# Performance work log

Hardware: AMD Instinct MI355X
Metric: run time of the kernel (lower is better)

## Reference

```python
import jax, jax.numpy as jnp
import numpy as np

N_NODES = 100000
N_EDGES = 6400000
D_FEAT = 128
HIDDEN = 16


def _gcn_conv(x, row, col, W, b, n):
    # PyG GCNConv: add self-loops, symmetric norm, message from row -> aggregated at col
    h = x @ W  # [N, out]
    loop = jnp.arange(n, dtype=row.dtype)
    r = jnp.concatenate([row, loop])
    c = jnp.concatenate([col, loop])
    ones = jnp.ones(r.shape[0], dtype=x.dtype)
    deg = jax.ops.segment_sum(ones, c, num_segments=n)  # in-degree incl. self-loop
    dinv = jnp.where(deg > 0, jax.lax.rsqrt(deg), 0.0)
    norm = dinv[r] * dinv[c]  # [E+N]
    msg = h[r] * norm[:, None]  # [E+N, out]
    out = jax.ops.segment_sum(msg, c, num_segments=n)
    return out + b


def setup_inputs() -> dict:
    key = jax.random.key(0)
    ks = jax.random.split(key, 8)
    x = jax.random.normal(ks[0], (N_NODES, D_FEAT), dtype=jnp.float32)
    edge_attr = jax.random.normal(ks[1], (N_EDGES, 1), dtype=jnp.float32)
    edge_row = jnp.sort(jax.random.randint(ks[2], (N_EDGES,), 0, N_NODES, dtype=jnp.int32)).astype(jnp.int64)
    edge_col = jax.random.randint(ks[3], (N_EDGES,), 0, N_NODES, dtype=jnp.int32).astype(jnp.int64)
    W1 = jax.random.normal(ks[4], (D_FEAT + 1, HIDDEN), dtype=jnp.float32) * (1.0 / np.sqrt(D_FEAT + 1))
    b1 = jnp.zeros((HIDDEN,), dtype=jnp.float32)
    W2 = jax.random.normal(ks[5], (HIDDEN, 1), dtype=jnp.float32) * (1.0 / np.sqrt(HIDDEN))
    b2 = jnp.zeros((1,), dtype=jnp.float32)
    return {"x": x, "edge_attr": edge_attr, "edge_row": edge_row, "edge_col": edge_col,
            "W1": W1, "b1": b1, "W2": W2, "b2": b2}


def reference(x, edge_attr, edge_row, edge_col, W1, b1, W2, b2):
    n = x.shape[0]
    # the original Python loop == segment-sum of edge_attr by source node (rows are sorted)
    x_edge = jax.ops.segment_sum(edge_attr, edge_row, num_segments=n)  # [N, 1]
    h = jnp.concatenate([x, x_edge], axis=1)  # [N, D+1]
    h = _gcn_conv(h, edge_row, edge_col, W1, b1, n)
    h = jax.nn.relu(h)
    # dropout is identity in eval mode
    out = _gcn_conv(h, edge_row, edge_col, W2, b2, n)  # [N, 1]
    return out
```

## Files before the change

kernel.cpp:

```cpp
#include <hip/hip_runtime.h>


#define D_FEAT 128
#define HIDDEN 16
#define TILE 8192
#define CAP 17408u
#define FXS 262144.0f
#define FXSI 3.814697265625e-06f

__device__ inline float bf2f(unsigned short u) {
    union { unsigned x; float f; } t; t.x = ((unsigned)u) << 16; return t.f;
}

__global__ __launch_bounds__(256) void k_init(float* xe, unsigned* gcur, int n, int nb) {
    int t = blockIdx.x * 256 + threadIdx.x;
    if (t < n) xe[t] = 0.f;
    if (t < nb) gcur[t * 16] = (unsigned)t * CAP;
}

__global__ __launch_bounds__(1024) void k_sortplace(const int* __restrict__ row,
                                                    const int* __restrict__ col,
                                                    const float* __restrict__ ea,
                                                    float* __restrict__ xe,
                                                    unsigned* __restrict__ gcur,
                                                    unsigned* __restrict__ ebufP,
                                                    int ne, int nb) {
    __shared__ unsigned stage[TILE];
    __shared__ unsigned short sbuck[TILE];
    __shared__ unsigned h[512], base_[512], cursor[512], gb_[512];
    __shared__ unsigned wsum[8];
    int tid = threadIdx.x;
    int lane = tid & 63;
    int w = tid >> 6;
    int tile0 = blockIdx.x * TILE;
    int cnt_t = min(TILE, ne - tile0);
    if (tid < 512) h[tid] = 0u;
    __syncthreads();
    int e0 = tile0 + tid * 8;
    int rr[8], cc[8];
    float aa[8];
    if (e0 + 7 < ne) {
        int4 r0 = *(const int4*)&row[e0];
        int4 r1 = *(const int4*)&row[e0 + 4];
        int4 c0 = *(const int4*)&col[e0];
        int4 c1 = *(const int4*)&col[e0 + 4];
        float4 a0 = *(const float4*)&ea[e0];
        float4 a1 = *(const float4*)&ea[e0 + 4];
        rr[0] = r0.x; rr[1] = r0.y; rr[2] = r0.z; rr[3] = r0.w;
        rr[4] = r1.x; rr[5] = r1.y; rr[6] = r1.z; rr[7] = r1.w;
        cc[0] = c0.x; cc[1] = c0.y; cc[2] = c0.z; cc[3] = c0.w;
        cc[4] = c1.x; cc[5] = c1.y; cc[6] = c1.z; cc[7] = c1.w;
        aa[0] = a0.x; aa[1] = a0.y; aa[2] = a0.z; aa[3] = a0.w;
        aa[4] = a1.x; aa[5] = a1.y; aa[6] = a1.z; aa[7] = a1.w;
    } else {
        #pragma unroll
        for (int k = 0; k < 8; ++k) {
            int e = e0 + k;
            if (e < ne) { rr[k] = row[e]; cc[k] = col[e]; aa[k] = ea[e]; }
            else        { rr[k] = -1; cc[k] = 0; aa[k] = 0.f; }
        }
    }
    #pragma unroll
    for (int k = 0; k < 8; ++k)
        if (rr[k] >= 0) atomicAdd(&h[cc[k] >> 8], 1u);
    int r_first = rr[0];
    float run = aa[0], lead = 0.f;
    #pragma unroll
    for (int k = 1; k < 8; ++k) {
        if (rr[k] == rr[k - 1]) run += aa[k];
        else {
            if (rr[k - 1] == r_first) lead = run;
            else if (rr[k - 1] >= 0) unsafeAtomicAdd(&xe[rr[k - 1]], run);
            run = aa[k];
        }
    }
    int r_last = rr[7];
    float trail = run;
    bool puref = (r_first == r_last);
    int rl_prev = __shfl_up(r_last, 1);
    bool m = (lane > 0) && (r_first == rl_prev);
    float s = trail;
    int f = (puref && m) ? 0 : 1;
    #pragma unroll
    for (int d = 1; d < 64; d <<= 1) {
        float su = __shfl_up(s, d);
        int fu = __shfl_up(f, d);
        if (lane >= d) {
            if (!f) s += su;
            f = f | fu;
        }
    }
    float o_prev = __shfl_up(s, 1);
    float inflow = m ? o_prev : 0.f;
    int rf_next = __shfl_down(r_first, 1);
    bool chain_end = (lane == 63) || (rf_next != r_last);
    if (!puref && r_first >= 0) unsafeAtomicAdd(&xe[r_first], lead + inflow);
    if (chain_end && r_last >= 0)
        unsafeAtomicAdd(&xe[r_last], trail + (puref ? inflow : 0.f));
    __syncthreads();
    unsigned hv = 0, sh = 0;
    if (tid < 512) {
        hv = h[tid];
        sh = hv;
        #pragma unroll
        for (int d = 1; d < 64; d <<= 1) {
            unsigned u = __shfl_up(sh, d);
            if (lane >= d) sh += u;
        }
        if (lane == 63) wsum[w] = sh;
    }
    __syncthreads();
    if (tid < 512) {
        unsigned woff = 0;
        #pragma unroll
        for (int i = 0; i < 8; ++i) woff += (i < w) ? wsum[i] : 0u;
        unsigned ex = sh + woff - hv;
        base_[tid] = ex;
        cursor[tid] = ex;
        if (tid < nb && hv) gb_[tid] = atomicAdd(&gcur[tid * 16], hv);
    }
    __syncthreads();
    #pragma unroll
    for (int k = 0; k < 8; ++k) {
        if (rr[k] >= 0) {
            int b = cc[k] >> 8;
            unsigned p = atomicAdd(&cursor[b], 1u);
            stage[p] = (((unsigned)(cc[k] & 255)) << 24) | (unsigned)rr[k];
            sbuck[p] = (unsigned short)b;
        }
    }
    __syncthreads();
    for (int t = tid; t < cnt_t; t += 1024) {
        unsigned b = sbuck[t];
        unsigned pos = gb_[b] + ((unsigned)t - base_[b]);
        if (pos < (b + 1u) * CAP) ebufP[pos] = stage[t];
    }
}

__global__ __launch_bounds__(512) void k_deghist(const unsigned* __restrict__ gcur,
                                                 const unsigned* __restrict__ ebufP,
                                                 unsigned* __restrict__ deg,
                                                 unsigned* __restrict__ stG, int n) {
    __shared__ unsigned dg[256];
    __shared__ unsigned wsum[4];
    int tid = threadIdx.x, b = blockIdx.x, lane = tid & 63;
    if (tid < 256) dg[tid] = 0u;
    __syncthreads();
    unsigned base = (unsigned)b * CAP;
    unsigned m = min(gcur[b * 16] - base, CAP);
    unsigned i = tid;
    for (; i + 1536 < m; i += 2048) {
        unsigned pk0 = ebufP[base + i];
        unsigned pk1 = ebufP[base + i + 512];
        unsigned pk2 = ebufP[base + i + 1024];
        unsigned pk3 = ebufP[base + i + 1536];
        atomicAdd(&dg[pk0 >> 24], 1u);
        atomicAdd(&dg[pk1 >> 24], 1u);
        atomicAdd(&dg[pk2 >> 24], 1u);
        atomicAdd(&dg[pk3 >> 24], 1u);
    }
    for (; i < m; i += 512) atomicAdd(&dg[ebufP[base + i] >> 24], 1u);
    __syncthreads();
    unsigned dval = 0, s = 0;
    if (tid < 256) {
        dval = dg[tid];
        s = dval;
        #pragma unroll
        for (int d = 1; d < 64; d <<= 1) {
            unsigned uu = __shfl_up(s, d);
            if (lane >= d) s += uu;
        }
        if (lane == 63) wsum[tid >> 6] = s;
    }
    __syncthreads();
    if (tid < 256) {
        int w = tid >> 6;
        unsigned woff = 0;
        #pragma unroll
        for (int i2 = 0; i2 < 4; ++i2) woff += (i2 < w) ? wsum[i2] : 0u;
        unsigned ex = s + woff - dval;
        int v = b * 256 + tid;
        if (v < n) { deg[v] = dval; stG[v] = base + ex; }
    }
}

__global__ __launch_bounds__(256) void k_gemm1(const float* __restrict__ x,
                                               const float* __restrict__ xe,
                                               const unsigned* __restrict__ deg,
                                               const float* __restrict__ W1,
                                               float* __restrict__ g,
                                               unsigned short* __restrict__ gb, int n) {
    __shared__ float WsT[16 * 132];
    __shared__ float xs[64 * 132];
    int tid = threadIdx.x;
    for (int idx = tid; idx < 129 * 16; idx += 256) {
        int k = idx >> 4, j = idx & 15;
        WsT[j * 132 + k] = W1[idx];
    }
    int n0 = blockIdx.x * 64;
    const float4* x4 = (const float4*)x;
    for (int idx = tid; idx < 64 * 32; idx += 256) {
        int r = idx >> 5, c = idx & 31;
        float4 v = (n0 + r < n) ? x4[(size_t)(n0 + r) * 32 + c]
                                : make_float4(0.f, 0.f, 0.f, 0.f);
        *(float4*)&xs[r * 132 + c * 4] = v;
    }
    if (tid < 64) {
        int r = tid;
        xs[r * 132 + 128] = (n0 + r < n) ? xe[n0 + r] : 0.f;
    }
    __syncthreads();
    int j  = tid & 15;
    int nb = tid >> 4;
    const float* wrow = &WsT[j * 132];
    for (int rep = 0; rep < 4; ++rep) {
        int nl = nb + (rep << 4);
        int node = n0 + nl;
        const float* xrow = &xs[nl * 132];
        float acc = 0.f;
        #pragma unroll
        for (int k = 0; k < 128; k += 4) {
            float4 xv = *(const float4*)&xrow[k];
            float4 wv = *(const float4*)&wrow[k];
            acc += xv.x * wv.x;
            acc += xv.y * wv.y;
            acc += xv.z * wv.z;
            acc += xv.w * wv.w;
        }
        acc += xrow[128] * wrow[128];
        if (node < n) {
            float v = acc * rsqrtf((float)deg[node] + 1.0f);
            g[(size_t)node * 16 + j] = v;
            union { float f; unsigned u; } cv; cv.f = v;
            unsigned r16 = (cv.u + 0x7FFFu + ((cv.u >> 16) & 1u)) >> 16;
            gb[(size_t)node * 16 + j] = (unsigned short)r16;
        }
    }
}

__global__ __launch_bounds__(512) void k_agg1s(const unsigned* __restrict__ gcur,
                                               const unsigned* __restrict__ ebufP,
                                               const unsigned* __restrict__ deg,
                                               const unsigned* __restrict__ stG,
                                               const unsigned* __restrict__ gu,
                                               const float* __restrict__ g,
                                               const float* __restrict__ b1,
                                               const float* __restrict__ W2,
                                               float* __restrict__ g2, int n) {
    __shared__ unsigned sorted[CAP];
    __shared__ unsigned dg[256], st[256], cur[256];
    int tid = threadIdx.x, b = blockIdx.x;
    unsigned base = (unsigned)b * CAP;
    unsigned m = min(gcur[b * 16] - base, CAP);
    if (tid < 256) {
        int v = b * 256 + tid;
        unsigned dval = (v < n) ? deg[v] : 0u;
        unsigned sv   = (v < n) ? stG[v] - base : 0u;
        dg[tid] = dval;
        st[tid] = sv;
        cur[tid] = sv;
    }
    __syncthreads();
    unsigned i = tid;
    for (; i + 1536 < m; i += 2048) {
        unsigned pk0 = ebufP[base + i];
        unsigned pk1 = ebufP[base + i + 512];
        unsigned pk2 = ebufP[base + i + 1024];
        unsigned pk3 = ebufP[base + i + 1536];
        unsigned p0 = atomicAdd(&cur[pk0 >> 24], 1u);
        unsigned p1 = atomicAdd(&cur[pk1 >> 24], 1u);
        unsigned p2 = atomicAdd(&cur[pk2 >> 24], 1u);
        unsigned p3 = atomicAdd(&cur[pk3 >> 24], 1u);
        if (p0 < CAP) sorted[p0] = pk0 & 0xFFFFFFu;
        if (p1 < CAP) sorted[p1] = pk1 & 0xFFFFFFu;
        if (p2 < CAP) sorted[p2] = pk2 & 0xFFFFFFu;
        if (p3 < CAP) sorted[p3] = pk3 & 0xFFFFFFu;
    }
    for (; i < m; i += 512) {
        unsigned pk = ebufP[base + i];
        unsigned p = atomicAdd(&cur[pk >> 24], 1u);
        if (p < CAP) sorted[p] = pk & 0xFFFFFFu;
    }
    __syncthreads();
    const uint4* gu4 = (const uint4*)gu;
    int grp = tid >> 4;
    int u = tid & 1;
    int oct = (tid >> 1) & 7;
    float4 bbA = ((const float4*)b1)[2 * u];
    float4 bbB = ((const float4*)b1)[2 * u + 1];
    float4 wwA = ((const float4*)W2)[2 * u];
    float4 wwB = ((const float4*)W2)[2 * u + 1];
    for (int it = 0; it < 8; ++it) {
        int c = it * 32 + grp;
        int v = b * 256 + c;
        if (v >= n) break;
        unsigned s0 = st[c], e0 = s0 + dg[c];
        float a0 = 0.f, a1 = 0.f, a2 = 0.f, a3 = 0.f;
        float a4 = 0.f, a5 = 0.f, a6 = 0.f, a7 = 0.f;
        float c0 = 0.f, c1 = 0.f, c2 = 0.f, c3 = 0.f;
        float c4 = 0.f, c5 = 0.f, c6 = 0.f, c7 = 0.f;
        unsigned q = s0 + oct;
        for (; q + 8 < e0; q += 16) {
            uint4 w0 = gu4[(size_t)sorted[q] * 2 + u];
            uint4 w1 = gu4[(size_t)sorted[q + 8] * 2 + u];
            a0 += bf2f((unsigned short)w0.x); a1 += bf2f((unsigned short)(w0.x >> 16));
            a2 += bf2f((unsigned short)w0.y); a3 += bf2f((unsigned short)(w0.y >> 16));
            a4 += bf2f((unsigned short)w0.z); a5 += bf2f((unsigned short)(w0.z >> 16));
            a6 += bf2f((unsigned short)w0.w); a7 += bf2f((unsigned short)(w0.w >> 16));
            c0 += bf2f((unsigned short)w1.x); c1 += bf2f((unsigned short)(w1.x >> 16));
            c2 += bf2f((unsigned short)w1.y); c3 += bf2f((unsigned short)(w1.y >> 16));
            c4 += bf2f((unsigned short)w1.z); c5 += bf2f((unsigned short)(w1.z >> 16));
            c6 += bf2f((unsigned short)w1.w); c7 += bf2f((unsigned short)(w1.w >> 16));
        }
        for (; q < e0; q += 8) {
            uint4 w0 = gu4[(size_t)sorted[q] * 2 + u];
            a0 += bf2f((unsigned short)w0.x); a1 += bf2f((unsigned short)(w0.x >> 16));
            a2 += bf2f((unsigned short)w0.y); a3 += bf2f((unsigned short)(w0.y >> 16));
            a4 += bf2f((unsigned short)w0.z); a5 += bf2f((unsigned short)(w0.z >> 16));
            a6 += bf2f((unsigned short)w0.w); a7 += bf2f((unsigned short)(w0.w >> 16));
        }
        a0 += c0; a1 += c1; a2 += c2; a3 += c3;
        a4 += c4; a5 += c5; a6 += c6; a7 += c7;
        #pragma unroll
        for (int d = 2; d <= 8; d <<= 1) {
            a0 += __shfl_xor(a0, d, 16);
            a1 += __shfl_xor(a1, d, 16);
            a2 += __shfl_xor(a2, d, 16);
            a3 += __shfl_xor(a3, d, 16);
            a4 += __shfl_xor(a4, d, 16);
            a5 += __shfl_xor(a5, d, 16);
            a6 += __shfl_xor(a6, d, 16);
            a7 += __shfl_xor(a7, d, 16);
        }
        float di = rsqrtf((float)dg[c] + 1.0f);
        float4 gA = ((const float4*)g)[(size_t)v * 4 + 2 * u];
        float4 gB = ((const float4*)g)[(size_t)v * 4 + 2 * u + 1];
        float v0 = fmaxf(di * (gA.x + a0) + bbA.x, 0.f);
        float v1 = fmaxf(di * (gA.y + a1) + bbA.y, 0.f);
        float v2 = fmaxf(di * (gA.z + a2) + bbA.z, 0.f);
        float v3 = fmaxf(di * (gA.w + a3) + bbA.w, 0.f);
        float v4 = fmaxf(di * (gB.x + a4) + bbB.x, 0.f);
        float v5 = fmaxf(di * (gB.y + a5) + bbB.y, 0.f);
        float v6 = fmaxf(di * (gB.z + a6) + bbB.z, 0.f);
        float v7 = fmaxf(di * (gB.w + a7) + bbB.w, 0.f);
        float prd = v0 * wwA.x + v1 * wwA.y + v2 * wwA.z + v3 * wwA.w
                  + v4 * wwB.x + v5 * wwB.y + v6 * wwB.z + v7 * wwB.w;
        prd += __shfl_xor(prd, 1, 16);
        if ((tid & 15) == 0) g2[v] = prd * di;
    }
}

__global__ __launch_bounds__(512) void k_agg2i(const unsigned* __restrict__ gcur,
                                               const unsigned* __restrict__ ebufP,
                                               const unsigned* __restrict__ deg,
                                               const float* __restrict__ g2,
                                               const float* __restrict__ b2,
                                               float* __restrict__ out, int n) {
    __shared__ int acc2[256];
    int tid = threadIdx.x, b = blockIdx.x;
    if (tid < 256) acc2[tid] = 0;
    __syncthreads();
    unsigned base = (unsigned)b * CAP;
    unsigned m = min(gcur[b * 16] - base, CAP);
    unsigned mt = m & ~3u;
    const uint4* eb4 = (const uint4*)(ebufP + base);
    for (unsigned t = tid; t * 4 + 3 < m; t += 512) {
        uint4 pk = eb4[t];
        float v0 = g2[pk.x & 0xFFFFFFu];
        float v1 = g2[pk.y & 0xFFFFFFu];
        float v2 = g2[pk.z & 0xFFFFFFu];
        float v3 = g2[pk.w & 0xFFFFFFu];
        atomicAdd(&acc2[pk.x >> 24], __float2int_rn(v0 * FXS));
        atomicAdd(&acc2[pk.y >> 24], __float2int_rn(v1 * FXS));
        atomicAdd(&acc2[pk.z >> 24], __float2int_rn(v2 * FXS));
        atomicAdd(&acc2[pk.w >> 24], __float2int_rn(v3 * FXS));
    }
    for (unsigned t = mt + tid; t < m; t += 512) {
        unsigned pk = ebufP[base + t];
        atomicAdd(&acc2[pk >> 24], __float2int_rn(g2[pk & 0xFFFFFFu] * FXS));
    }
    __syncthreads();
    if (tid < 256) {
        int v = b * 256 + tid;
        if (v < n) {
            float a = (float)acc2[tid] * FXSI;
            float di = rsqrtf((float)deg[v] + 1.0f);
            out[v] = di * (g2[v] + a) + b2[0];
        }
    }
}

extern "C" void kernel_launch(void* const* d_in, const int* in_sizes, int n_in,
                              void* d_out, int out_size, void* d_ws, size_t ws_size,
                              hipStream_t stream) {
    const float* x   = (const float*)d_in[0];
    const float* ea  = (const float*)d_in[1];
    const int*   row = (const int*)d_in[2];
    const int*   col = (const int*)d_in[3];
    const float* W1  = (const float*)d_in[4];
    const float* b1  = (const float*)d_in[5];
    const float* W2  = (const float*)d_in[6];
    const float* b2  = (const float*)d_in[7];
    float* out = (float*)d_out;

    int n  = in_sizes[0] / D_FEAT;
    int ne = in_sizes[2];
    int nb = (n + 255) >> 8;

    float* ws   = (float*)d_ws;
    float* xe   = ws;
    float* g    = ws + (size_t)n;
    float* g2   = ws + (size_t)17 * n;
    unsigned short* gbuf = (unsigned short*)(ws + (size_t)18 * n);
    unsigned* deg  = (unsigned*)(ws + (size_t)26 * n);
    unsigned* stG  = deg + (size_t)n;
    unsigned* gcur = stG + (size_t)n;
    unsigned* ebufP = gcur + (size_t)nb * 16;

    dim3 blk(256);
    int g_node = (n + 255) / 256;
    int g_tile = (ne + TILE - 1) / TILE;
    int g_gemm = (n + 63) / 64;

    k_init<<<g_node, blk, 0, stream>>>(xe, gcur, n, nb);
    k_sortplace<<<g_tile, 1024, 0, stream>>>(row, col, ea, xe, gcur, ebufP, ne, nb);
    k_deghist<<<nb, 512, 0, stream>>>(gcur, ebufP, deg, stG, n);
    k_gemm1<<<g_gemm, blk, 0, stream>>>(x, xe, deg, W1, g, gbuf, n);
    k_agg1s<<<nb, 512, 0, stream>>>(gcur, ebufP, deg, stG, (const unsigned*)gbuf, g, b1, W2, g2, n);
    k_agg2i<<<nb, 512, 0, stream>>>(gcur, ebufP, deg, g2, b2, out, n);
}
```

Baseline: 257.0 us.

## Run the x@W1 GEMM concurrently with edge bucketing in one fused kernel

The edge sort/place kernel and the 128-wide part of the first GEMM now share one launch, with blocks assigned by bid%3 to either sorting or a 64-node GEMM tile. The GEMM result no longer depends on the degree, so the x_edge column, the degree normalisation and the bf16 packing move into the degree-histogram kernel as a per-node epilogue. This drops one launch and lets the memory-bound GEMM overlap the atomic-heavy sort. The cost is a union shared-memory footprint sized for the larger role, an extra read-modify-write pass over g, and role imbalance if the two grid counts differ.

```diff
diff --git a/kernel.cpp b/kernel.cpp
--- a/kernel.cpp
+++ b/kernel.cpp
@@ -18,133 +18,200 @@
     if (t < nb) gcur[t * 16] = (unsigned)t * CAP;
 }
 
-__global__ __launch_bounds__(1024) void k_sortplace(const int* __restrict__ row,
-                                                    const int* __restrict__ col,
-                                                    const float* __restrict__ ea,
-                                                    float* __restrict__ xe,
-                                                    unsigned* __restrict__ gcur,
-                                                    unsigned* __restrict__ ebufP,
-                                                    int ne, int nb) {
-    __shared__ unsigned stage[TILE];
-    __shared__ unsigned short sbuck[TILE];
-    __shared__ unsigned h[512], base_[512], cursor[512], gb_[512];
-    __shared__ unsigned wsum[8];
+__global__ __launch_bounds__(1024) void k_sortgemm(const int* __restrict__ row,
+                                                   const int* __restrict__ col,
+                                                   const float* __restrict__ ea,
+                                                   float* __restrict__ xe,
+                                                   unsigned* __restrict__ gcur,
+                                                   unsigned* __restrict__ ebufP,
+                                                   int ne, int nb,
+                                                   const float* __restrict__ x,
+                                                   const float* __restrict__ W1,
+                                                   float* __restrict__ g, int n) {
+    __shared__ union {
+        struct {
+            unsigned stage[TILE];
+            unsigned short sbuck[TILE];
+            unsigned h[512], base_[512], cursor[512], gb_[512];
+            unsigned wsum[8];
+        } sp;
+        struct {
+            float WsT[16 * 132];
+            float xs[64 * 132];
+        } gm;
+    } u;
+    int bid = blockIdx.x;
     int tid = threadIdx.x;
-    int lane = tid & 63;
-    int w = tid >> 6;
-    int tile0 = blockIdx.x * TILE;
-    int cnt_t = min(TILE, ne - tile0);
-    if (tid < 512) h[tid] = 0u;
-    __syncthreads();
-    int e0 = tile0 + tid * 8;
-    int rr[8], cc[8];
-    float aa[8];
-    if (e0 + 7 < ne) {
-        int4 r0 = *(const int4*)&row[e0];
-        int4 r1 = *(const int4*)&row[e0 + 4];
-        int4 c0 = *(const int4*)&col[e0];
-        int4 c1 = *(const int4*)&col[e0 + 4];
-        float4 a0 = *(const float4*)&ea[e0];
-        float4 a1 = *(const float4*)&ea[e0 + 4];
-        rr[0] = r0.x; rr[1] = r0.y; rr[2] = r0.z; rr[3] = r0.w;
-        rr[4] = r1.x; rr[5] = r1.y; rr[6] = r1.z; rr[7] = r1.w;
-        cc[0] = c0.x; cc[1] = c0.y; cc[2] = c0.z; cc[3] = c0.w;
-        cc[4] = c1.x; cc[5] = c1.y; cc[6] = c1.z; cc[7] = c1.w;
-        aa[0] = a0.x; aa[1] = a0.y; aa[2] = a0.z; aa[3] = a0.w;
-        aa[4] = a1.x; aa[5] = a1.y; aa[6] = a1.z; aa[7] = a1.w;
+    int role = bid % 3;
+    if (role == 0) {
+        int sb = bid / 3;
+        int ntile = (ne + TILE - 1) / TILE;
+        if (sb >= ntile) return;
+        unsigned* stage = u.sp.stage;
+        unsigned short* sbuck = u.sp.sbuck;
+        unsigned* h = u.sp.h;
+        unsigned* base_ = u.sp.base_;
+        unsigned* cursor = u.sp.cursor;
+        unsigned* gb_ = u.sp.gb_;
+        unsigned* wsum = u.sp.wsum;
+        int lane = tid & 63;
+        int w = tid >> 6;
+        int tile0 = sb * TILE;
+        int cnt_t = min(TILE, ne - tile0);
+        if (tid < 512) h[tid] = 0u;
+        __syncthreads();
+        int e0 = tile0 + tid * 8;
+        int rr[8], cc[8];
+        float aa[8];
+        if (e0 + 7 < ne) {
+            int4 r0 = *(const int4*)&row[e0];
+            int4 r1 = *(const int4*)&row[e0 + 4];
+            int4 c0 = *(const int4*)&col[e0];
+            int4 c1 = *(const int4*)&col[e0 + 4];
+            float4 a0 = *(const float4*)&ea[e0];
+            float4 a1 = *(const float4*)&ea[e0 + 4];
+            rr[0] = r0.x; rr[1] = r0.y; rr[2] = r0.z; rr[3] = r0.w;
+            rr[4] = r1.x; rr[5] = r1.y; rr[6] = r1.z; rr[7] = r1.w;
+            cc[0] = c0.x; cc[1] = c0.y; cc[2] = c0.z; cc[3] = c0.w;
+            cc[4] = c1.x; cc[5] = c1.y; cc[6] = c1.z; cc[7] = c1.w;
+            aa[0] = a0.x; aa[1] = a0.y; aa[2] = a0.z; aa[3] = a0.w;
+            aa[4] = a1.x; aa[5] = a1.y; aa[6] = a1.z; aa[7] = a1.w;
+        } else {
+            #pragma unroll
+            for (int k = 0; k < 8; ++k) {
+                int e = e0 + k;
+                if (e < ne) { rr[k] = row[e]; cc[k] = col[e]; aa[k] = ea[e]; }
+                else        { rr[k] = -1; cc[k] = 0; aa[k] = 0.f; }
+            }
+        }
+        #pragma unroll
+        for (int k = 0; k < 8; ++k)
+            if (rr[k] >= 0) atomicAdd(&h[cc[k] >> 8], 1u);
+        int r_first = rr[0];
+        float run = aa[0], lead = 0.f;
+        #pragma unroll
+        for (int k = 1; k < 8; ++k) {
+            if (rr[k] == rr[k - 1]) run += aa[k];
+            else {
+                if (rr[k - 1] == r_first) lead = run;
+                else if (rr[k - 1] >= 0) unsafeAtomicAdd(&xe[rr[k - 1]], run);
+                run = aa[k];
+            }
+        }
+        int r_last = rr[7];
+        float trail = run;
+        bool puref = (r_first == r_last);
+        int rl_prev = __shfl_up(r_last, 1);
+        bool m = (lane > 0) && (r_first == rl_prev);
+        float s = trail;
+        int f = (puref && m) ? 0 : 1;
+        #pragma unroll
+        for (int d = 1; d < 64; d <<= 1) {
+            float su = __shfl_up(s, d);
+            int fu = __shfl_up(f, d);
+            if (lane >= d) {
+                if (!f) s += su;
+                f = f | fu;
+            }
+        }
+        float o_prev = __shfl_up(s, 1);
+        float inflow = m ? o_prev : 0.f;
+        int rf_next = __shfl_down(r_first, 1);
+        bool chain_end = (lane == 63) || (rf_next != r_last);
+        if (!puref && r_first >= 0) unsafeAtomicAdd(&xe[r_first], lead + inflow);
+        if (chain_end && r_last >= 0)
+            unsafeAtomicAdd(&xe[r_last], trail + (puref ? inflow : 0.f));
+        __syncthreads();
+        unsigned hv = 0, sh = 0;
+        if (tid < 512) {
+            hv = h[tid];
+            sh = hv;
+            #pragma unroll
+            for (int d = 1; d < 64; d <<= 1) {
+                unsigned uu = __shfl_up(sh, d);
+                if (lane >= d) sh += uu;
+            }
+            if (lane == 63) wsum[w] = sh;
+        }
+        __syncthreads();
+        if (tid < 512) {
+            unsigned woff = 0;
+            #pragma unroll
+            for (int i = 0; i < 8; ++i) woff += (i < w) ? wsum[i] : 0u;
+            unsigned ex = sh + woff - hv;
+            base_[tid] = ex;
+            cursor[tid] = ex;
+            if (tid < nb && hv) gb_[tid] = atomicAdd(&gcur[tid * 16], hv);
+        }
+        __syncthreads();
+        #pragma unroll
+        for (int k = 0; k < 8; ++k) {
+            if (rr[k] >= 0) {
+                int b = cc[k] >> 8;
+                unsigned p = atomicAdd(&cursor[b], 1u);
+                stage[p] = (((unsigned)(cc[k] & 255)) << 24) | (unsigned)rr[k];
+                sbuck[p] = (unsigned short)b;
+            }
+        }
+        __syncthreads();
+        for (int t = tid; t < cnt_t; t += 1024) {
+            unsigned b = sbuck[t];
+            unsigned pos = gb_[b] + ((unsigned)t - base_[b]);
+            if (pos < (b + 1u) * CAP) ebufP[pos] = stage[t];
+        }
     } else {
-        #pragma unroll
-        for (int k = 0; k < 8; ++k) {
-            int e = e0 + k;
-            if (e < ne) { rr[k] = row[e]; cc[k] = col[e]; aa[k] = ea[e]; }
-            else        { rr[k] = -1; cc[k] = 0; aa[k] = 0.f; }
-        }
-    }
-    #pragma unroll
-    for (int k = 0; k < 8; ++k)
-        if (rr[k] >= 0) atomicAdd(&h[cc[k] >> 8], 1u);
-    int r_first = rr[0];
-    float run = aa[0], lead = 0.f;
-    #pragma unroll
-    for (int k = 1; k < 8; ++k) {
-        if (rr[k] == rr[k - 1]) run += aa[k];
-        else {
-            if (rr[k - 1] == r_first) lead = run;
-            else if (rr[k - 1] >= 0) unsafeAtomicAdd(&xe[rr[k - 1]], run);
-            run = aa[k];
-        }
-    }
-    int r_last = rr[7];
-    float trail = run;
-    bool puref = (r_first == r_last);
-    int rl_prev = __shfl_up(r_last, 1);
-    bool m = (lane > 0) && (r_first == rl_prev);
-    float s = trail;
-    int f = (puref && m) ? 0 : 1;
-    #pragma unroll
-    for (int d = 1; d < 64; d <<= 1) {
-        float su = __shfl_up(s, d);
-        int fu = __shfl_up(f, d);
-        if (lane >= d) {
-            if (!f) s += su;
-            f = f | fu;
-        }
-    }
-    float o_prev = __shfl_up(s, 1);
-    float inflow = m ? o_prev : 0.f;
-    int rf_next = __shfl_down(r_first, 1);
-    bool chain_end = (lane == 63) || (rf_next != r_last);
-    if (!puref && r_first >= 0) unsafeAtomicAdd(&xe[r_first], lead + inflow);
-    if (chain_end && r_last >= 0)
-        unsafeAtomicAdd(&xe[r_last], trail + (puref ? inflow : 0.f));
-    __syncthreads();
-    unsigned hv = 0, sh = 0;
-    if (tid < 512) {
-        hv = h[tid];
-        sh = hv;
-        #pragma unroll
-        for (int d = 1; d < 64; d <<= 1) {
-            unsigned u = __shfl_up(sh, d);
-            if (lane >= d) sh += u;
-        }
-        if (lane == 63) wsum[w] = sh;
-    }
-    __syncthreads();
-    if (tid < 512) {
-        unsigned woff = 0;
-        #pragma unroll
-        for (int i = 0; i < 8; ++i) woff += (i < w) ? wsum[i] : 0u;
-        unsigned ex = sh + woff - hv;
-        base_[tid] = ex;
-        cursor[tid] = ex;
-        if (tid < nb && hv) gb_[tid] = atomicAdd(&gcur[tid * 16], hv);
-    }
-    __syncthreads();
-    #pragma unroll
-    for (int k = 0; k < 8; ++k) {
-        if (rr[k] >= 0) {
-            int b = cc[k] >> 8;
-            unsigned p = atomicAdd(&cursor[b], 1u);
-            stage[p] = (((unsigned)(cc[k] & 255)) << 24) | (unsigned)rr[k];
-            sbuck[p] = (unsigned short)b;
-        }
-    }
-    __syncthreads();
-    for (int t = tid; t < cnt_t; t += 1024) {
-        unsigned b = sbuck[t];
-        unsigned pos = gb_[b] + ((unsigned)t - base_[b]);
-        if (pos < (b + 1u) * CAP) ebufP[pos] = stage[t];
+        int gb = (bid / 3) * 2 + role - 1;
+        int ngemm = (n + 63) / 64;
+        if (gb >= ngemm) return;
+        float* WsT = u.gm.WsT;
+        float* xs  = u.gm.xs;
+        int n0 = gb * 64;
+        for (int idx = tid; idx < 129 * 16; idx += 1024) {
+            int k = idx >> 4, j = idx & 15;
+            WsT[j * 132 + k] = W1[idx];
+        }
+        const float4* x4 = (const float4*)x;
+        for (int idx = tid; idx < 64 * 32; idx += 1024) {
+            int r = idx >> 5, c = idx & 31;
+            float4 v = (n0 + r < n) ? x4[(size_t)(n0 + r) * 32 + c]
+                                    : make_float4(0.f, 0.f, 0.f, 0.f);
+            *(float4*)&xs[r * 132 + c * 4] = v;
+        }
+        __syncthreads();
+        int j  = tid & 15;
+        int nl = tid >> 4;
+        int node = n0 + nl;
+        const float* xrow = &xs[nl * 132];
+        const float* wrow = &WsT[j * 132];
+        float acc = 0.f;
+        #pragma unroll
+        for (int k = 0; k < 128; k += 4) {
+            float4 xv = *(const float4*)&xrow[k];
+            float4 wv = *(const float4*)&wrow[k];
+            acc += xv.x * wv.x;
+            acc += xv.y * wv.y;
+            acc += xv.z * wv.z;
+            acc += xv.w * wv.w;
+        }
+        if (node < n) g[(size_t)node * 16 + j] = acc;
     }
 }
 
 __global__ __launch_bounds__(512) void k_deghist(const unsigned* __restrict__ gcur,
                                                  const unsigned* __restrict__ ebufP,
                                                  unsigned* __restrict__ deg,
-                                                 unsigned* __restrict__ stG, int n) {
+                                                 unsigned* __restrict__ stG,
+                                                 const float* __restrict__ xe,
+                                                 const float* __restrict__ W1,
+                                                 float* __restrict__ g,
+                                                 unsigned short* __restrict__ gbuf, int n) {
     __shared__ unsigned dg[256];
     __shared__ unsigned wsum[4];
+    __shared__ float w128[16];
+    __shared__ float ddinv[256];
     int tid = threadIdx.x, b = blockIdx.x, lane = tid & 63;
     if (tid < 256) dg[tid] = 0u;
+    if (tid >= 256 && tid < 272) w128[tid - 256] = W1[128 * 16 + (tid - 256)];
     __syncthreads();
     unsigned base = (unsigned)b * CAP;
     unsigned m = min(gcur[b * 16] - base, CAP);
@@ -181,60 +248,34 @@
         unsigned ex = s + woff - dval;
         int v = b * 256 + tid;
         if (v < n) { deg[v] = dval; stG[v] = base + ex; }
-    }
-}
-
-__global__ __launch_bounds__(256) void k_gemm1(const float* __restrict__ x,
-                                               const float* __restrict__ xe,
-                                               const unsigned* __restrict__ deg,
-                                               const float* __restrict__ W1,
-                                               float* __restrict__ g,
-                                               unsigned short* __restrict__ gb, int n) {
-    __shared__ float WsT[16 * 132];
-    __shared__ float xs[64 * 132];
-    int tid = threadIdx.x;
-    for (int idx = tid; idx < 129 * 16; idx += 256) {
-        int k = idx >> 4, j = idx & 15;
-        WsT[j * 132 + k] = W1[idx];
-    }
-    int n0 = blockIdx.x * 64;
-    const float4* x4 = (const float4*)x;
-    for (int idx = tid; idx < 64 * 32; idx += 256) {
-        int r = idx >> 5, c = idx & 31;
-        float4 v = (n0 + r < n) ? x4[(size_t)(n0 + r) * 32 + c]
-                                : make_float4(0.f, 0.f, 0.f, 0.f);
-        *(float4*)&xs[r * 132 + c * 4] = v;
-    }
-    if (tid < 64) {
-        int r = tid;
-        xs[r * 132 + 128] = (n0 + r < n) ? xe[n0 + r] : 0.f;
-    }
-    __syncthreads();
-    int j  = tid & 15;
-    int nb = tid >> 4;
-    const float* wrow = &WsT[j * 132];
-    for (int rep = 0; rep < 4; ++rep) {
-        int nl = nb + (rep << 4);
-        int node = n0 + nl;
-        const float* xrow = &xs[nl * 132];
-        float acc = 0.f;
-        #pragma unroll
-        for (int k = 0; k < 128; k += 4) {
-            float4 xv = *(const float4*)&xrow[k];
-            float4 wv = *(const float4*)&wrow[k];
-            acc += xv.x * wv.x;
-            acc += xv.y * wv.y;
-            acc += xv.z * wv.z;
-            acc += xv.w * wv.w;
-        }
-        acc += xrow[128] * wrow[128];
-        if (node < n) {
-            float v = acc * rsqrtf((float)deg[node] + 1.0f);
-            g[(size_t)node * 16 + j] = v;
-            union { float f; unsigned u; } cv; cv.f = v;
-            unsigned r16 = (cv.u + 0x7FFFu + ((cv.u >> 16) & 1u)) >> 16;
-            gb[(size_t)node * 16 + j] = (unsigned short)r16;
-        }
+        ddinv[tid] = rsqrtf((float)dval + 1.0f);
+    }
+    __syncthreads();
+    float* gbk = g + (size_t)b * 4096;
+    unsigned short* gbk16 = gbuf + (size_t)b * 4096;
+    for (int q = tid; q < 1024; q += 512) {
+        int nl = q >> 2;
+        int v = b * 256 + nl;
+        if (v >= n) break;
+        float4 r = *(const float4*)&gbk[q * 4];
+        float xv = xe[v];
+        float di = ddinv[nl];
+        int j0 = (q & 3) * 4;
+        r.x = (r.x + xv * w128[j0 + 0]) * di;
+        r.y = (r.y + xv * w128[j0 + 1]) * di;
+        r.z = (r.z + xv * w128[j0 + 2]) * di;
+        r.w = (r.w + xv * w128[j0 + 3]) * di;
+        *(float4*)&gbk[q * 4] = r;
+        union { float f; unsigned u; } c0, c1, c2, c3;
+        c0.f = r.x; c1.f = r.y; c2.f = r.z; c3.f = r.w;
+        unsigned r0 = (c0.u + 0x7FFFu + ((c0.u >> 16) & 1u)) >> 16;
+        unsigned r1 = (c1.u + 0x7FFFu + ((c1.u >> 16) & 1u)) >> 16;
+        unsigned r2 = (c2.u + 0x7FFFu + ((c2.u >> 16) & 1u)) >> 16;
+        unsigned r3 = (c3.u + 0x7FFFu + ((c3.u >> 16) & 1u)) >> 16;
+        uint2 pk;
+        pk.x = r0 | (r1 << 16);
+        pk.y = r2 | (r3 << 16);
+        *(uint2*)&gbk16[q * 4] = pk;
     }
 }
 
@@ -421,11 +462,13 @@
     int g_node = (n + 255) / 256;
     int g_tile = (ne + TILE - 1) / TILE;
     int g_gemm = (n + 63) / 64;
+    int slots  = g_tile > (g_gemm + 1) / 2 ? g_tile : (g_gemm + 1) / 2;
+    int g_fat  = slots * 3;
 
     k_init<<<g_node, blk, 0, stream>>>(xe, gcur, n, nb);
-    k_sortplace<<<g_tile, 1024, 0, stream>>>(row, col, ea, xe, gcur, ebufP, ne, nb);
-    k_deghist<<<nb, 512, 0, stream>>>(gcur, ebufP, deg, stG, n);
-    k_gemm1<<<g_gemm, blk, 0, stream>>>(x, xe, deg, W1, g, gbuf, n);
+    k_sortgemm<<<g_fat, 1024, 0, stream>>>(row, col, ea, xe, gcur, ebufP, ne, nb,
+                                           x, W1, g, n);
+    k_deghist<<<nb, 512, 0, stream>>>(gcur, ebufP, deg, stG, xe, W1, g, gbuf, n);
     k_agg1s<<<nb, 512, 0, stream>>>(gcur, ebufP, deg, stG, (const unsigned*)gbuf, g, b1, W2, g2, n);
     k_agg2i<<<nb, 512, 0, stream>>>(gcur, ebufP, deg, g2, b2, out, n);
 }
```

Result: faster. 236.3 us, median of 2 (-8.0%).
